# Optimization experiments

Measured on AMD Instinct MI355X. Metric: run time of the kernel, lower is better.

The kernel has to match this reference:

```python
import jax, jax.numpy as jnp
import numpy as np

CURV = 1.0          # manifold curvature c
HEADS = 4
HEAD_DIM = 32       # (dim-1) // heads = 128 // 4
SCALE = HEAD_DIM ** -0.5
EPS = 1e-7

N_NODES = 50000
N_EDGES = 800000
D = 128             # tangent feature dim (dim - 1)


def log_origin(x, c):
    """Lorentz log map at the origin o=(1/sqrt(c),0,...); returns spatial (d) part of tangent."""
    sc = jnp.sqrt(c)
    x0 = x[..., 0]
    xs = x[..., 1:]
    norm = jnp.sqrt(jnp.sum(xs * xs, axis=-1) + EPS)         # (N,)
    dist = jnp.arccosh(jnp.maximum(sc * x0, 1.0 + EPS)) / sc  # (N,)
    return (dist / norm)[..., None] * xs                      # (N, d)


def exp_origin(vs, c):
    """Lorentz exp map at origin of tangent vector (0, vs); returns point (N, d+1)."""
    sc = jnp.sqrt(c)
    r = jnp.sqrt(jnp.sum(vs * vs, axis=-1) + EPS)  # (N,)
    arg = sc * r
    x0 = jnp.cosh(arg) / sc
    xs = (jnp.sinh(arg) / arg)[..., None] * vs
    return jnp.concatenate([x0[..., None], xs], axis=-1)


def setup_inputs() -> dict:
    key = jax.random.key(0)
    k1, k2, k3, k4, k5, k6, k7 = jax.random.split(key, 7)
    # valid hyperboloid points: x0 = sqrt(1/c + ||xs||^2)
    xs = 0.5 * jax.random.normal(k1, (N_NODES, D), dtype=jnp.float32)
    x0 = jnp.sqrt(1.0 / CURV + jnp.sum(xs * xs, axis=-1, keepdims=True))
    x = jnp.concatenate([x0, xs], axis=-1)  # (N, d+1)
    edge_index = jax.random.randint(k2, (2, N_EDGES), 0, N_NODES, dtype=jnp.int64)
    s = D ** -0.5
    Wq = s * jax.random.normal(k3, (D, D), dtype=jnp.float32)
    Wk = s * jax.random.normal(k4, (D, D), dtype=jnp.float32)
    Wv = s * jax.random.normal(k5, (D, D), dtype=jnp.float32)
    Wo = s * jax.random.normal(k6, (D, D), dtype=jnp.float32)
    bo = jnp.zeros((D,), dtype=jnp.float32)
    return {"x": x, "edge_index": edge_index, "Wq": Wq, "Wk": Wk, "Wv": Wv, "Wo": Wo, "bo": bo}


def reference(x, edge_index, Wq, Wk, Wv, Wo, bo):
    N = x.shape[0]
    row, col = edge_index[0], edge_index[1]
    # map to tangent space at origin, drop the (zero) time component
    x_tan = log_origin(x, CURV)                       # (N, d)
    Q = (x_tan @ Wq.T).reshape(N, HEADS, HEAD_DIM)
    K = (x_tan @ Wk.T).reshape(N, HEADS, HEAD_DIM)
    V = (x_tan @ Wv.T).reshape(N, HEADS, HEAD_DIM)
    # per-edge attention logits, grouped softmax over incoming edges of each target node (col)
    scores = jnp.einsum('ehd,ehd->eh', Q[col], K[row]) * SCALE   # (E, H)
    m = jax.ops.segment_max(scores, col, num_segments=N)         # (N, H)
    e = jnp.exp(scores - m[col])
    denom = jax.ops.segment_sum(e, col, num_segments=N)          # (N, H)
    att = e / denom[col]                                         # (E, H)
    # weighted scatter-sum of values
    agg = jax.ops.segment_sum(att[..., None] * V[row], col, num_segments=N)  # (N, H, hd)
    agg = agg.reshape(N, HEADS * HEAD_DIM)
    out = agg @ Wo.T + bo                                        # (N, d)
    # lift back: prepend zero time component, exp map at origin
    return exp_origin(out, CURV)                                 # (N, d+1)
```

## Files before the change

kernel.cpp:

```cpp
#include <hip/hip_runtime.h>
#include <hip/hip_fp8.h>
#include <math.h>

#define EPS 1e-7f
#define SCALE 0.17677669529663687f
#define MAXDEG 64

typedef _Float16 half2v __attribute__((ext_vector_type(2)));
typedef _Float16 f16x4 __attribute__((ext_vector_type(4)));
typedef _Float16 f16x8 __attribute__((ext_vector_type(8)));
typedef float f32x4 __attribute__((ext_vector_type(4)));

__device__ __forceinline__ void gload16(const void* g, void* l) {
  __builtin_amdgcn_global_load_lds(
      (const __attribute__((address_space(1))) unsigned int*)g,
      (__attribute__((address_space(3))) unsigned int*)l, 16, 0, 0);
}

__device__ __forceinline__ float f8tof(unsigned char u) {
  __hip_fp8_e4m3 h;
  h.__x = (__hip_fp8_storage_t)u;
  return (float)h;
}
__device__ __forceinline__ unsigned char ftof8(float f) {
  __hip_fp8_e4m3 h(f);
  return (unsigned char)h.__x;
}

__global__ __launch_bounds__(256) void prep_kernel(
    const float* __restrict__ x,
    const float* __restrict__ Wq, const float* __restrict__ Wk,
    const float* __restrict__ Wv, const float* __restrict__ Wo,
    _Float16* __restrict__ Wc, _Float16* __restrict__ Wof,
    _Float16* __restrict__ xt, int* __restrict__ cnt, int N) {
  int b = blockIdx.x;
  if (b < 256) {
    int o = b * 256 + threadIdx.x;
    int j = o >> 7;
    int i = o & 127;
    if (j < 384) {
      const float* W = (j < 128) ? Wq : (j < 256) ? Wk : Wv;
      Wc[o] = (_Float16)W[(j & 127) * 128 + i];
    } else {
      Wof[(j - 384) * 128 + i] = (_Float16)Wo[(j - 384) * 128 + i];
    }
    return;
  }
  int node = (b - 256) * 4 + (threadIdx.x >> 6);
  if (node >= N) return;
  int lane = threadIdx.x & 63;
  float2 xs = *reinterpret_cast<const float2*>(&x[(size_t)node * 129 + 1 + lane * 2]);
  float ss = fmaf(xs.x, xs.x, xs.y * xs.y);
#pragma unroll
  for (int o = 32; o >= 1; o >>= 1) ss += __shfl_xor(ss, o, 64);
  float norm = sqrtf(ss + EPS);
  float x0 = x[(size_t)node * 129];
  float dist = acoshf(fmaxf(x0, 1.0f + EPS));
  float sc = dist / norm;
  half2v h;
  h.x = (_Float16)(sc * xs.x);
  h.y = (_Float16)(sc * xs.y);
  *reinterpret_cast<half2v*>(&xt[(size_t)node * 128 + lane * 2]) = h;
  if (lane == 0) cnt[node] = 0;
}

template <int NCHUNKS, int MODE>
__global__ __launch_bounds__(256, 3) void gemm_mfma(
    const _Float16* __restrict__ A,
    const _Float16* __restrict__ B,
    void* __restrict__ C0, void* __restrict__ C1,
    const float* __restrict__ bias, int M,
    const int* __restrict__ col, const int* __restrict__ row,
    int* __restrict__ cnt, int* __restrict__ rml, int E) {
  int bid;
  if (MODE == 0) {
    if ((blockIdx.x & 1) == 0) {
      int stride = (gridDim.x >> 1) * 256;
      for (int e = (blockIdx.x >> 1) * 256 + threadIdx.x; e < E; e += stride) {
        int c = col[e];
        int pos = atomicAdd(&cnt[c], 1);
        if (pos < MAXDEG) rml[c * MAXDEG + pos] = row[e];
      }
      return;
    }
    bid = blockIdx.x >> 1;
  } else {
    bid = blockIdx.x;
  }

  __shared__ _Float16 As[64 * 128];
  __shared__ _Float16 Bs[128 * 128];
  const int tid = threadIdx.x;
  const int wave = tid >> 6;
  const int lane = tid & 63;
  const int wm = wave >> 1, wn = wave & 1;
  const int lrow = lane & 15, q = lane >> 4;
  const int m0 = bid * 64;

#pragma unroll
  for (int j = 0; j < 4; j++) {
    int slot0 = (j * 4 + wave) * 64;
    int p = slot0 + lane;
    int m = p >> 4;
    int kcl = (p & 15) ^ (m & 15);
    int msrc = m0 + m;
    if (msrc > M - 1) msrc = M - 1;
    gload16(A + (size_t)msrc * 128 + kcl * 8, (char*)As + (size_t)slot0 * 16);
  }

  f32x4 acc[2][4];
  for (int c = 0; c < NCHUNKS; c++) {
#pragma unroll
    for (int j = 0; j < 8; j++) {
      int slot0 = (j * 4 + wave) * 64;
      int p = slot0 + lane;
      int n = p >> 4;
      int kcl = (p & 15) ^ (n & 15);
      gload16(B + ((size_t)(c * 128 + n)) * 128 + kcl * 8, (char*)Bs + (size_t)slot0 * 16);
    }
    __syncthreads();

#pragma unroll
    for (int mt = 0; mt < 2; mt++)
#pragma unroll
      for (int nt = 0; nt < 4; nt++) acc[mt][nt] = (f32x4)0.f;

    const f16x8* Av = (const f16x8*)As;
    const f16x8* Bv = (const f16x8*)Bs;
#pragma unroll
    for (int s = 0; s < 4; s++) {
      int kc = s * 4 + q;
      f16x8 af[2], bf[4];
#pragma unroll
      for (int mt = 0; mt < 2; mt++) {
        int m = wm * 32 + mt * 16 + lrow;
        af[mt] = Av[m * 16 + (kc ^ (m & 15))];
      }
#pragma unroll
      for (int nt = 0; nt < 4; nt++) {
        int n = wn * 64 + nt * 16 + lrow;
        bf[nt] = Bv[n * 16 + (kc ^ (n & 15))];
      }
#pragma unroll
      for (int mt = 0; mt < 2; mt++)
#pragma unroll
        for (int nt = 0; nt < 4; nt++)
          acc[mt][nt] = __builtin_amdgcn_mfma_f32_16x16x32_f16(af[mt], bf[nt], acc[mt][nt], 0, 0, 0);
    }

    if (MODE == 0) {
#pragma unroll
      for (int mt = 0; mt < 2; mt++) {
#pragma unroll
        for (int reg = 0; reg < 4; reg++) {
          int rg = m0 + wm * 32 + mt * 16 + q * 4 + reg;
          if (rg < M) {
#pragma unroll
            for (int nt = 0; nt < 4; nt++) {
              int cl = wn * 64 + nt * 16 + lrow;
              float v = acc[mt][nt][reg];
              if (c == 0) {
                ((_Float16*)C0)[(size_t)rg * 128 + cl] = (_Float16)v;
              } else {
                int h = cl >> 5, j = cl & 31;
                int idx = (h * 8 + (j >> 2)) * 8 + ((c == 2) ? 4 : 0) + (j & 3);
                ((unsigned char*)C1)[(size_t)rg * 256 + idx] = ftof8(v);
              }
            }
          }
        }
      }
      if (c + 1 < NCHUNKS) __syncthreads();
    }
  }

  if (MODE == 1) {
    float* out = (float*)C0;
    __syncthreads();
    float* rsum = (float*)As;
#pragma unroll
    for (int mt = 0; mt < 2; mt++)
#pragma unroll
      for (int nt = 0; nt < 4; nt++) {
        int cl = wn * 64 + nt * 16 + lrow;
        float b = bias[cl];
#pragma unroll
        for (int reg = 0; reg < 4; reg++) acc[mt][nt][reg] += b;
      }
#pragma unroll
    for (int mt = 0; mt < 2; mt++) {
#pragma unroll
      for (int reg = 0; reg < 4; reg++) {
        float s4 = 0.f;
#pragma unroll
        for (int nt = 0; nt < 4; nt++) s4 = fmaf(acc[mt][nt][reg], acc[mt][nt][reg], s4);
#pragma unroll
        for (int o = 8; o >= 1; o >>= 1) s4 += __shfl_xor(s4, o, 16);
        if (lrow == 0) rsum[(wm * 32 + mt * 16 + q * 4 + reg) * 2 + wn] = s4;
      }
    }
    __syncthreads();
#pragma unroll
    for (int mt = 0; mt < 2; mt++) {
#pragma unroll
      for (int reg = 0; reg < 4; reg++) {
        int rl = wm * 32 + mt * 16 + q * 4 + reg;
        int rg = m0 + rl;
        if (rg < M) {
          float tot = rsum[rl * 2] + rsum[rl * 2 + 1];
          float r = sqrtf(tot + EPS);
          float s = sinhf(r) / r;
#pragma unroll
          for (int nt = 0; nt < 4; nt++) {
            int cl = wn * 64 + nt * 16 + lrow;
            out[(size_t)rg * 129 + 1 + cl] = s * acc[mt][nt][reg];
          }
          if (wn == 0 && lrow == 0) out[(size_t)rg * 129] = coshf(r);
        }
      }
    }
  }
}

__global__ __launch_bounds__(256) void attn_kernel(
    const _Float16* __restrict__ Qb,
    const unsigned char* __restrict__ KVI,
    const int* __restrict__ rml, const int* __restrict__ cnt,
    _Float16* __restrict__ agg, int N) {
  int node = blockIdx.x * 4 + (threadIdx.x >> 6);
  if (node >= N) return;
  int lane = threadIdx.x & 63;
  int par = lane >> 5;
  int hd = lane & 31;
  int qoff = hd * 4;
  f16x4 qh = *reinterpret_cast<const f16x4*>(Qb + (size_t)node * 128 + qoff);
  float q0 = (float)qh[0], q1 = (float)qh[1], q2 = (float)qh[2], q3 = (float)qh[3];
  int deg = cnt[node];
  if (deg > MAXDEG) deg = MAXDEG;
  const int* el = rml + (size_t)node * MAXDEG;
  float l = 0.f, av0 = 0.f, av1 = 0.f, av2 = 0.f, av3 = 0.f;

  auto dot = [&](uint2 w, float& p, float& v0, float& v1, float& v2, float& v3) {
    unsigned kx = w.x, vx = w.y;
    float k0 = f8tof(kx & 255), k1 = f8tof((kx >> 8) & 255);
    float k2 = f8tof((kx >> 16) & 255), k3 = f8tof(kx >> 24);
    v0 = f8tof(vx & 255); v1 = f8tof((vx >> 8) & 255);
    v2 = f8tof((vx >> 16) & 255); v3 = f8tof(vx >> 24);
    p = fmaf(q0, k0, fmaf(q1, k1, fmaf(q2, k2, q3 * k3)));
  };

  int i = 0;
  for (; i + 8 <= deg; i += 8) {
    int rA = el[i + par], rB = el[i + 2 + par], rC = el[i + 4 + par], rD = el[i + 6 + par];
    uint2 wA = *reinterpret_cast<const uint2*>(KVI + (size_t)rA * 256 + hd * 8);
    uint2 wB = *reinterpret_cast<const uint2*>(KVI + (size_t)rB * 256 + hd * 8);
    uint2 wC = *reinterpret_cast<const uint2*>(KVI + (size_t)rC * 256 + hd * 8);
    uint2 wD = *reinterpret_cast<const uint2*>(KVI + (size_t)rD * 256 + hd * 8);
    float pA, a4, a5, a6, a7;
    float pB, b4, b5, b6, b7;
    float pC, c4, c5, c6, c7;
    float pD, d4, d5, d6, d7;
    dot(wA, pA, a4, a5, a6, a7);
    dot(wB, pB, b4, b5, b6, b7);
    dot(wC, pC, c4, c5, c6, c7);
    dot(wD, pD, d4, d5, d6, d7);
#pragma unroll
    for (int o = 4; o >= 1; o >>= 1) {
      pA += __shfl_xor(pA, o, 8);
      pB += __shfl_xor(pB, o, 8);
      pC += __shfl_xor(pC, o, 8);
      pD += __shfl_xor(pD, o, 8);
    }
    float eA = __expf(pA * SCALE);
    float eB = __expf(pB * SCALE);
    float eC = __expf(pC * SCALE);
    float eD = __expf(pD * SCALE);
    l += (eA + eB) + (eC + eD);
    av0 = fmaf(eA, a4, av0); av0 = fmaf(eB, b4, av0);
    av1 = fmaf(eA, a5, av1); av1 = fmaf(eB, b5, av1);
    av2 = fmaf(eA, a6, av2); av2 = fmaf(eB, b6, av2);
    av3 = fmaf(eA, a7, av3); av3 = fmaf(eB, b7, av3);
    av0 = fmaf(eC, c4, av0); av0 = fmaf(eD, d4, av0);
    av1 = fmaf(eC, c5, av1); av1 = fmaf(eD, d5, av1);
    av2 = fmaf(eC, c6, av2); av2 = fmaf(eD, d6, av2);
    av3 = fmaf(eC, c7, av3); av3 = fmaf(eD, d7, av3);
  }
  for (; i + 2 <= deg; i += 2) {
    int rA = el[i + par];
    uint2 wA = *reinterpret_cast<const uint2*>(KVI + (size_t)rA * 256 + hd * 8);
    float pA, a4, a5, a6, a7;
    dot(wA, pA, a4, a5, a6, a7);
#pragma unroll
    for (int o = 4; o >= 1; o >>= 1) pA += __shfl_xor(pA, o, 8);
    float eA = __expf(pA * SCALE);
    l += eA;
    av0 = fmaf(eA, a4, av0);
    av1 = fmaf(eA, a5, av1);
    av2 = fmaf(eA, a6, av2);
    av3 = fmaf(eA, a7, av3);
  }
  if (i < deg) {
    int r = el[i];
    uint2 wA = *reinterpret_cast<const uint2*>(KVI + (size_t)r * 256 + hd * 8);
    float pA, a4, a5, a6, a7;
    dot(wA, pA, a4, a5, a6, a7);
#pragma unroll
    for (int o = 4; o >= 1; o >>= 1) pA += __shfl_xor(pA, o, 8);
    float e = __expf(pA * SCALE) * (par ? 0.f : 1.f);
    l += e;
    av0 = fmaf(e, a4, av0);
    av1 = fmaf(e, a5, av1);
    av2 = fmaf(e, a6, av2);
    av3 = fmaf(e, a7, av3);
  }
  l += __shfl_xor(l, 32, 64);
  av0 += __shfl_xor(av0, 32, 64);
  av1 += __shfl_xor(av1, 32, 64);
  av2 += __shfl_xor(av2, 32, 64);
  av3 += __shfl_xor(av3, 32, 64);
  if (par == 0) {
    float inv = (l > 0.f) ? 1.0f / l : 0.f;
    f16x4 o4;
    o4[0] = (_Float16)(av0 * inv);
    o4[1] = (_Float16)(av1 * inv);
    o4[2] = (_Float16)(av2 * inv);
    o4[3] = (_Float16)(av3 * inv);
    *reinterpret_cast<f16x4*>(agg + (size_t)node * 128 + qoff) = o4;
  }
}

extern "C" void kernel_launch(void* const* d_in, const int* in_sizes, int n_in,
                              void* d_out, int out_size, void* d_ws, size_t ws_size,
                              hipStream_t stream) {
  const float* x = (const float*)d_in[0];
  const int* ei = (const int*)d_in[1];
  const float* Wq = (const float*)d_in[2];
  const float* Wk = (const float*)d_in[3];
  const float* Wv = (const float*)d_in[4];
  const float* Wo = (const float*)d_in[5];
  const float* bo = (const float*)d_in[6];
  float* out = (float*)d_out;

  const int N = in_sizes[0] / 129;
  const int E = in_sizes[1] / 2;
  const int* row = ei;
  const int* col = ei + E;

  char* ws = (char*)d_ws;
  size_t off = 0;
  auto alloc = [&](size_t bytes) -> void* {
    off = (off + 255) & ~(size_t)255;
    void* p = ws + off;
    off += bytes;
    return p;
  };
  _Float16* xtan = (_Float16*)alloc((size_t)N * 128 * 2);
  _Float16* qbuf = (_Float16*)alloc((size_t)N * 128 * 2);
  unsigned char* kvi = (unsigned char*)alloc((size_t)N * 256);
  int* rml       = (int*)alloc((size_t)N * MAXDEG * 4);
  _Float16* Wc   = (_Float16*)alloc(384 * 128 * 2);
  _Float16* Wof  = (_Float16*)alloc(128 * 128 * 2);
  int* cnt       = (int*)alloc((size_t)(N + 1) * 4);

  const int gemm_nb = (N + 63) / 64;

  prep_kernel<<<256 + (N + 3) / 4, 256, 0, stream>>>(x, Wq, Wk, Wv, Wo, Wc, Wof,
                                                     xtan, cnt, N);
  gemm_mfma<3, 0><<<gemm_nb * 2, 256, 0, stream>>>(xtan, Wc, qbuf, kvi, nullptr, N,
                                                   col, row, cnt, rml, E);
  attn_kernel<<<(N + 3) / 4, 256, 0, stream>>>(qbuf, kvi, rml, cnt, xtan, N);
  gemm_mfma<1, 1><<<gemm_nb, 256, 0, stream>>>(xtan, Wof, out, nullptr, bo, N,
                                               nullptr, nullptr, nullptr, nullptr, 0);
}
```

Measured before the change: 201.0 us.

## Stage GEMM epilogue through LDS, keep A fragments in registers, use 16-bit edge lists

The QKV GEMM loads its A tile into registers once and reuses its shared memory for B. It prefetches the next B chunk while the previous chunk's results are written out. Results are staged in a swizzled LDS buffer so global stores become 16-byte or 8-byte coalesced writes instead of scattered 2-byte and 1-byte stores. The neighbour lists switch from int32 to uint16 to halve index traffic in the attention kernel; this assumes fewer than 65536 nodes.

```diff
diff --git a/kernel.cpp b/kernel.cpp
--- a/kernel.cpp
+++ b/kernel.cpp
@@ -71,15 +71,15 @@
     void* __restrict__ C0, void* __restrict__ C1,
     const float* __restrict__ bias, int M,
     const int* __restrict__ col, const int* __restrict__ row,
-    int* __restrict__ cnt, int* __restrict__ rml, int E) {
+    int* __restrict__ cnt, unsigned short* __restrict__ rml, int E) {
   int bid;
   if (MODE == 0) {
     if ((blockIdx.x & 1) == 0) {
       int stride = (gridDim.x >> 1) * 256;
-      for (int e = (blockIdx.x >> 1) * 256 + threadIdx.x; e < E; e += stride) {
+      for (int e = (blockIdx.x >> 1) * 256 + (int)threadIdx.x; e < E; e += stride) {
         int c = col[e];
         int pos = atomicAdd(&cnt[c], 1);
-        if (pos < MAXDEG) rml[c * MAXDEG + pos] = row[e];
+        if (pos < MAXDEG) rml[(size_t)c * MAXDEG + pos] = (unsigned short)row[e];
       }
       return;
     }
@@ -88,8 +88,8 @@
     bid = blockIdx.x;
   }
 
-  __shared__ _Float16 As[64 * 128];
   __shared__ _Float16 Bs[128 * 128];
+  __shared__ __align__(16) unsigned char Cs[16384];
   const int tid = threadIdx.x;
   const int wave = tid >> 6;
   const int lane = tid & 63;
@@ -105,11 +105,26 @@
     int kcl = (p & 15) ^ (m & 15);
     int msrc = m0 + m;
     if (msrc > M - 1) msrc = M - 1;
-    gload16(A + (size_t)msrc * 128 + kcl * 8, (char*)As + (size_t)slot0 * 16);
-  }
-
-  f32x4 acc[2][4];
-  for (int c = 0; c < NCHUNKS; c++) {
+    gload16(A + (size_t)msrc * 128 + kcl * 8, (char*)Bs + (size_t)slot0 * 16);
+  }
+  __syncthreads();
+
+  f16x8 afr[2][4];
+  {
+    const f16x8* Av = (const f16x8*)Bs;
+#pragma unroll
+    for (int mt = 0; mt < 2; mt++) {
+      int m = wm * 32 + mt * 16 + lrow;
+#pragma unroll
+      for (int s = 0; s < 4; s++) {
+        int kc = s * 4 + q;
+        afr[mt][s] = Av[m * 16 + (kc ^ (m & 15))];
+      }
+    }
+  }
+  __syncthreads();
+
+  auto stageB = [&](int c) {
 #pragma unroll
     for (int j = 0; j < 8; j++) {
       int slot0 = (j * 4 + wave) * 64;
@@ -118,6 +133,11 @@
       int kcl = (p & 15) ^ (n & 15);
       gload16(B + ((size_t)(c * 128 + n)) * 128 + kcl * 8, (char*)Bs + (size_t)slot0 * 16);
     }
+  };
+  stageB(0);
+
+  f32x4 acc[2][4];
+  for (int c = 0; c < NCHUNKS; c++) {
     __syncthreads();
 
 #pragma unroll
@@ -125,17 +145,11 @@
 #pragma unroll
       for (int nt = 0; nt < 4; nt++) acc[mt][nt] = (f32x4)0.f;
 
-    const f16x8* Av = (const f16x8*)As;
     const f16x8* Bv = (const f16x8*)Bs;
 #pragma unroll
     for (int s = 0; s < 4; s++) {
       int kc = s * 4 + q;
-      f16x8 af[2], bf[4];
-#pragma unroll
-      for (int mt = 0; mt < 2; mt++) {
-        int m = wm * 32 + mt * 16 + lrow;
-        af[mt] = Av[m * 16 + (kc ^ (m & 15))];
-      }
+      f16x8 bf[4];
 #pragma unroll
       for (int nt = 0; nt < 4; nt++) {
         int n = wn * 64 + nt * 16 + lrow;
@@ -145,39 +159,77 @@
       for (int mt = 0; mt < 2; mt++)
 #pragma unroll
         for (int nt = 0; nt < 4; nt++)
-          acc[mt][nt] = __builtin_amdgcn_mfma_f32_16x16x32_f16(af[mt], bf[nt], acc[mt][nt], 0, 0, 0);
+          acc[mt][nt] = __builtin_amdgcn_mfma_f32_16x16x32_f16(afr[mt][s], bf[nt], acc[mt][nt], 0, 0, 0);
     }
 
     if (MODE == 0) {
-#pragma unroll
-      for (int mt = 0; mt < 2; mt++) {
-#pragma unroll
-        for (int reg = 0; reg < 4; reg++) {
-          int rg = m0 + wm * 32 + mt * 16 + q * 4 + reg;
-          if (rg < M) {
+      if (c == 0) {
+#pragma unroll
+        for (int mt = 0; mt < 2; mt++)
+#pragma unroll
+          for (int reg = 0; reg < 4; reg++) {
+            int r = wm * 32 + mt * 16 + q * 4 + reg;
+            int sw = ((r >> 2) & 3) << 5;
 #pragma unroll
             for (int nt = 0; nt < 4; nt++) {
               int cl = wn * 64 + nt * 16 + lrow;
-              float v = acc[mt][nt][reg];
-              if (c == 0) {
-                ((_Float16*)C0)[(size_t)rg * 128 + cl] = (_Float16)v;
-              } else {
-                int h = cl >> 5, j = cl & 31;
-                int idx = (h * 8 + (j >> 2)) * 8 + ((c == 2) ? 4 : 0) + (j & 3);
-                ((unsigned char*)C1)[(size_t)rg * 256 + idx] = ftof8(v);
-              }
+              *(_Float16*)(Cs + r * 256 + ((cl * 2) ^ sw)) = (_Float16)acc[mt][nt][reg];
             }
           }
+      } else {
+        unsigned char* cb = Cs + ((c == 2) ? 8192 : 0);
+#pragma unroll
+        for (int mt = 0; mt < 2; mt++)
+#pragma unroll
+          for (int reg = 0; reg < 4; reg++) {
+            int r = wm * 32 + mt * 16 + q * 4 + reg;
+            int sw = ((r >> 2) & 3) << 5;
+#pragma unroll
+            for (int nt = 0; nt < 4; nt++) {
+              int cl = wn * 64 + nt * 16 + lrow;
+              cb[r * 128 + (cl ^ sw)] = ftof8(acc[mt][nt][reg]);
+            }
+          }
+      }
+    }
+    __syncthreads();
+    if (c + 1 < NCHUNKS) stageB(c + 1);
+    if (MODE == 0) {
+      if (c == 0) {
+#pragma unroll
+        for (int it = 0; it < 4; it++) {
+          int off = it * 4096 + tid * 16;
+          int r = off >> 8;
+          int bo = off & 255;
+          int sw = ((r >> 2) & 3) << 5;
+          uint4 v = *(const uint4*)(Cs + r * 256 + (bo ^ sw));
+          int rg = m0 + r;
+          if (rg < M) *(uint4*)((char*)C0 + (size_t)rg * 256 + bo) = v;
         }
-      }
-      if (c + 1 < NCHUNKS) __syncthreads();
+      } else if (c == 2) {
+#pragma unroll
+        for (int it = 0; it < 8; it++) {
+          int off = it * 2048 + tid * 8;
+          int r = off >> 8;
+          int u4 = (off & 255) >> 1;
+          int sw = ((r >> 2) & 3) << 5;
+          unsigned kw = *(const unsigned*)(Cs + r * 128 + (u4 ^ sw));
+          unsigned vw = *(const unsigned*)(Cs + 8192 + r * 128 + (u4 ^ sw));
+          int rg = m0 + r;
+          if (rg < M) {
+            uint2 o;
+            o.x = kw;
+            o.y = vw;
+            *(uint2*)((char*)C1 + (size_t)rg * 256 + (off & 255)) = o;
+          }
+        }
+      }
     }
   }
 
   if (MODE == 1) {
     float* out = (float*)C0;
-    __syncthreads();
-    float* rsum = (float*)As;
+    float* rsum = (float*)Cs;
 #pragma unroll
     for (int mt = 0; mt < 2; mt++)
 #pragma unroll
@@ -225,7 +277,7 @@
 __global__ __launch_bounds__(256) void attn_kernel(
     const _Float16* __restrict__ Qb,
     const unsigned char* __restrict__ KVI,
-    const int* __restrict__ rml, const int* __restrict__ cnt,
+    const unsigned short* __restrict__ rml, const int* __restrict__ cnt,
     _Float16* __restrict__ agg, int N) {
   int node = blockIdx.x * 4 + (threadIdx.x >> 6);
   if (node >= N) return;
@@ -237,7 +289,7 @@
   float q0 = (float)qh[0], q1 = (float)qh[1], q2 = (float)qh[2], q3 = (float)qh[3];
   int deg = cnt[node];
   if (deg > MAXDEG) deg = MAXDEG;
-  const int* el = rml + (size_t)node * MAXDEG;
+  const unsigned short* el = rml + (size_t)node * MAXDEG;
   float l = 0.f, av0 = 0.f, av1 = 0.f, av2 = 0.f, av3 = 0.f;
 
   auto dot = [&](uint2 w, float& p, float& v0, float& v1, float& v2, float& v3) {
@@ -357,7 +409,7 @@
   _Float16* xtan = (_Float16*)alloc((size_t)N * 128 * 2);
   _Float16* qbuf = (_Float16*)alloc((size_t)N * 128 * 2);
   unsigned char* kvi = (unsigned char*)alloc((size_t)N * 256);
-  int* rml       = (int*)alloc((size_t)N * MAXDEG * 4);
+  unsigned short* rml = (unsigned short*)alloc((size_t)N * MAXDEG * 2);
   _Float16* Wc   = (_Float16*)alloc(384 * 128 * 2);
   _Float16* Wof  = (_Float16*)alloc(128 * 128 * 2);
   int* cnt       = (int*)alloc((size_t)(N + 1) * 4);
```

New measurement: 195.6 us. -2.7%, faster.
